# Optimization experiments

Measured on AMD Instinct MI355X. Metric: run time of the kernel, lower is better.

Reference implementation:

```python
import jax, jax.numpy as jnp
import numpy as np

B = 4096
IN_DIM = 256
OUT_DIM = 256
COND_DIM = 128
HID = 512
HYPER_OUT = IN_DIM * OUT_DIM  # 65536


def setup_inputs() -> dict:
    key = jax.random.key(0)
    ks = jax.random.split(key, 8)

    def xavier(k, shape):
        fan_in, fan_out = shape[0], shape[1]
        std = np.sqrt(2.0 / (fan_in + fan_out))
        return jax.random.normal(k, shape, dtype=jnp.float32) * std

    return {
        "input_h": jax.random.normal(ks[0], (B, IN_DIM), dtype=jnp.float32),
        "condition_z": jax.random.normal(ks[1], (B, COND_DIM), dtype=jnp.float32),
        # hypernet: Linear(COND_DIM, HID) -> ReLU -> Linear(HID, HYPER_OUT)
        "W1": xavier(ks[2], (COND_DIM, HID)),
        "b1": jnp.zeros((HID,), dtype=jnp.float32),
        "W2": xavier(ks[3], (HID, HYPER_OUT)),
        "b2": jnp.zeros((HYPER_OUT,), dtype=jnp.float32),
        # static bias (use_bias=True, generate_bias=False)
        "bias": jnp.zeros((1, OUT_DIM), dtype=jnp.float32),
    }


def reference(input_h, condition_z, W1, b1, W2, b2, bias):
    # HyperNet MLP generates per-sample weight matrix
    hyp = jax.nn.relu(condition_z @ W1 + b1)          # [B, HID]
    weight_S = hyp @ W2 + b2                          # [B, IN*OUT]  (1 GB intermediate)
    weight_S = weight_S.reshape(-1, IN_DIM, OUT_DIM)  # [B, IN, OUT]
    # batched matmul: [B,1,IN] x [B,IN,OUT] -> [B,OUT]
    out = jnp.einsum("bi,bio->bo", input_h, weight_S)
    return out + bias
```

## Files before the change

### kernel.cpp

```cpp
#include <hip/hip_runtime.h>
#include <hip/hip_bf16.h>
#include <stdint.h>


typedef _Float16 f16x8 __attribute__((ext_vector_type(8)));
typedef _Float16 f16x4 __attribute__((ext_vector_type(4)));
typedef float    f32x4 __attribute__((ext_vector_type(4)));

#define KTILES     2052
#define TILE_BYTES 32768
#define HB_OFF     (9u*1024u*1024u)
#define BP_OFF     (12u*1024u*1024u)

__global__ void k_init_out(const float* __restrict__ bias, float* __restrict__ out) {
    int idx = blockIdx.x * 256 + threadIdx.x;
    out[idx] = bias[idx & 255];
}

__global__ void k_hcast(const float* __restrict__ h, _Float16* __restrict__ hb) {
    int i = (blockIdx.x * 256 + threadIdx.x) * 8;
    f32x4 a = *(const f32x4*)(h + i);
    f32x4 b = *(const f32x4*)(h + i + 4);
    f16x8 v;
    v[0] = (_Float16)a[0]; v[1] = (_Float16)a[1]; v[2] = (_Float16)a[2]; v[3] = (_Float16)a[3];
    v[4] = (_Float16)b[0]; v[5] = (_Float16)b[1]; v[6] = (_Float16)b[2]; v[7] = (_Float16)b[3];
    *(f16x8*)(hb + i) = v;
}

__global__ void k_hypT(const float* __restrict__ z, const float* __restrict__ W1,
                       const float* __restrict__ b1, float* __restrict__ hypT) {
    int blk = blockIdx.x;
    int t   = threadIdx.x;
    if (blk == 128) {
#pragma unroll
        for (int r = 0; r < 8; ++r) hypT[(size_t)512*4096 + r*512 + t] = 1.0f;
        return;
    }
    __shared__ float zs[32][128];
    int b0 = blk * 32;
#pragma unroll
    for (int u = 0; u < 8; ++u) {
        int idx = u * 512 + t;
        zs[idx >> 7][idx & 127] = z[b0 * 128 + idx];
    }
    __syncthreads();
    float acc[32];
    float bk = b1[t];
#pragma unroll
    for (int b = 0; b < 32; ++b) acc[b] = bk;
    for (int c = 0; c < 128; ++c) {
        float w = W1[c * 512 + t];
#pragma unroll
        for (int b = 0; b < 32; ++b) acc[b] = fmaf(zs[b][c], w, acc[b]);
    }
    float* dst = hypT + (size_t)t * 4096 + b0;
#pragma unroll
    for (int v = 0; v < 8; ++v) {
        f32x4 o;
#pragma unroll
        for (int q = 0; q < 4; ++q) {
            float a = acc[v * 4 + q];
            o[q] = a > 0.f ? a : 0.f;
        }
        *(f32x4*)(dst + v * 4) = o;
    }
}

__global__ void k_pack(const float* __restrict__ W2, const float* __restrict__ b2,
                       _Float16* __restrict__ Bp) {
    __shared__ char tile[TILE_BYTES];
    int t   = blockIdx.x;
    int tid = threadIdx.x;
    long row0 = (long)t * 64;
    const float* src = (t < 2048) ? (W2 + row0 * 256) : (b2 + (row0 - 131072) * 256);
#pragma unroll
    for (int u = 0; u < 16; ++u) {
        int f = (u * 256 + tid) * 4;
        f32x4 v = *(const f32x4*)(src + f);
        int kk = f >> 8;
        int o0 = f & 255;
#pragma unroll
        for (int j = 0; j < 4; ++j) {
            int o = o0 + j;
            int addr = (o * 128 + kk * 2) ^ ((o & 7) << 4);
            *(_Float16*)(tile + addr) = (_Float16)v[j];
        }
    }
    __syncthreads();
    char* dst = (char*)Bp + (size_t)t * TILE_BYTES;
#pragma unroll
    for (int v = 0; v < 8; ++v) {
        int off = (v * 256 + tid) * 16;
        *(f32x4*)(dst + off) = *(const f32x4*)(tile + off);
    }
}

__global__ __launch_bounds__(512, 1) void k_gemm(
        const _Float16* __restrict__ hb, const float* __restrict__ hypT,
        const _Float16* __restrict__ Bp, float* __restrict__ out) {
    __shared__ char smem[114688];

    const int tid  = threadIdx.x;
    const int lane = tid & 63;
    const int wid  = tid >> 6;
    const int l15  = lane & 15, lg = lane >> 4;

    const int bid = blockIdx.x;
    const int s   = bid & 7;
    const int mt  = bid >> 3;
    const int k0  = s * 64;
    const int row_base = mt * 128;
    const int NT  = (s == 7) ? 260 : 256;

    _Float16* shyp = (_Float16*)(smem + 98304);

#pragma unroll
    for (int u = 0; u < 4; ++u) {
        int f  = (u * 512 + tid) * 4;
        int kk = f >> 7;
        int r  = f & 127;
        f32x4 v = *(const f32x4*)(hypT + (size_t)(k0 + kk) * 4096 + row_base + r);
        f16x4 o;
        o[0] = (_Float16)v[0]; o[1] = (_Float16)v[1];
        o[2] = (_Float16)v[2]; o[3] = (_Float16)v[3];
        *(f16x4*)(shyp + kk * 128 + r) = o;
    }

    auto tile_of = [&](int idx) {
        return (idx < 256) ? ((k0 + (idx & 63)) * 4 + (idx >> 6)) : (2048 + idx - 256);
    };
    auto stage = [&](int slot, int t) {
        const char* gsrc = (const char*)Bp + (size_t)t * TILE_BYTES + wid * 4096 + lane * 16;
        char* ldst = smem + slot * 32768 + wid * 4096;
#pragma unroll
        for (int q = 0; q < 4; ++q)
            __builtin_amdgcn_global_load_lds(
                (const __attribute__((address_space(1))) void*)(gsrc + q * 1024),
                (__attribute__((address_space(3))) void*)(ldst + q * 1024), 16, 0, 0);
    };

    stage(0, tile_of(0));
    stage(1, tile_of(1));
    __syncthreads();

    f32x4 acc[8][2];
#pragma unroll
    for (int i = 0; i < 8; ++i)
#pragma unroll
        for (int j = 0; j < 2; ++j)
#pragma unroll
            for (int q = 0; q < 4; ++q) acc[i][j][q] = 0.0f;

    int slot = 0;

    for (int G = 0; G < 8; ++G) {
        if (G >= 4 && s != 7) break;
        const int niter = (G < 4) ? 64 : 1;

        f16x8 af[8][2];
#pragma unroll
        for (int mf = 0; mf < 8; ++mf)
#pragma unroll
            for (int ks = 0; ks < 2; ++ks)
                af[mf][ks] = *(const f16x8*)(hb + (size_t)(row_base + mf * 16 + l15) * 256
                                             + (G & 3) * 64 + ks * 32 + lg * 8);

        for (int jj = 0; jj < niter; ++jj) {
            const int idx = (G < 4) ? G * 64 + jj : 256 + (G - 4);

            if (idx + 2 < NT) {
                int st = (slot + 2 >= 3) ? slot - 1 : slot + 2;
                stage(st, tile_of(idx + 2));
            }
            if (idx + 2 < NT)      asm volatile("s_waitcnt vmcnt(8)" ::: "memory");
            else if (idx + 1 < NT) asm volatile("s_waitcnt vmcnt(4)" ::: "memory");
            else                   asm volatile("s_waitcnt vmcnt(0)" ::: "memory");

            const char* sB = smem + slot * 32768;
            f16x8 b0[2], b1[2];
#pragma unroll
            for (int nf = 0; nf < 2; ++nf) {
                int col = wid * 32 + nf * 16 + l15;
                int swz = (col & 7) << 4;
                b0[nf] = *(const f16x8*)(sB + ((col * 128 + lg * 16) ^ swz));
                b1[nf] = *(const f16x8*)(sB + ((col * 128 + 64 + lg * 16) ^ swz));
            }
            _Float16 sch[8];
            if (idx < 256) {
#pragma unroll
                for (int mf = 0; mf < 8; ++mf)
                    sch[mf] = shyp[jj * 128 + mf * 16 + l15];
            } else {
#pragma unroll
                for (int mf = 0; mf < 8; ++mf) sch[mf] = (_Float16)1.0f;
            }

            __builtin_amdgcn_s_setprio(1);
#pragma unroll
            for (int mf = 0; mf < 8; ++mf) {
                f16x8 as0 = af[mf][0] * sch[mf];
                f16x8 as1 = af[mf][1] * sch[mf];
                acc[mf][0] = __builtin_amdgcn_mfma_f32_16x16x32_f16(as0, b0[0], acc[mf][0], 0, 0, 0);
                acc[mf][1] = __builtin_amdgcn_mfma_f32_16x16x32_f16(as0, b0[1], acc[mf][1], 0, 0, 0);
                acc[mf][0] = __builtin_amdgcn_mfma_f32_16x16x32_f16(as1, b1[0], acc[mf][0], 0, 0, 0);
                acc[mf][1] = __builtin_amdgcn_mfma_f32_16x16x32_f16(as1, b1[1], acc[mf][1], 0, 0, 0);
            }
            __builtin_amdgcn_s_setprio(0);

            slot = (slot + 1 >= 3) ? 0 : slot + 1;
        }
    }

#pragma unroll
    for (int mf = 0; mf < 8; ++mf)
#pragma unroll
        for (int nf = 0; nf < 2; ++nf) {
            int col = wid * 32 + nf * 16 + l15;
#pragma unroll
            for (int q = 0; q < 4; ++q) {
                int row = row_base + mf * 16 + lg * 4 + q;
                atomicAdd(&out[row * 256 + col], acc[mf][nf][q]);
            }
        }
}

extern "C" void kernel_launch(void* const* d_in, const int* in_sizes, int n_in,
                              void* d_out, int out_size, void* d_ws, size_t ws_size,
                              hipStream_t stream) {
    const float* h    = (const float*)d_in[0];
    const float* z    = (const float*)d_in[1];
    const float* W1   = (const float*)d_in[2];
    const float* b1   = (const float*)d_in[3];
    const float* W2   = (const float*)d_in[4];
    const float* b2   = (const float*)d_in[5];
    const float* bias = (const float*)d_in[6];
    float* out = (float*)d_out;

    float*     hypT = (float*)d_ws;
    _Float16*  hb   = (_Float16*)((char*)d_ws + HB_OFF);
    _Float16*  Bp   = (_Float16*)((char*)d_ws + BP_OFF);

    k_pack    <<<KTILES, 256, 0, stream>>>(W2, b2, Bp);
    k_hypT    <<<129,    512, 0, stream>>>(z, W1, b1, hypT);
    k_hcast   <<<512,    256, 0, stream>>>(h, hb);
    k_init_out<<<4096,   256, 0, stream>>>(bias, out);
    k_gemm    <<<256,    512, 0, stream>>>(hb, hypT, Bp, out);
}
```

Baseline: 316.2 us.

## Deepen B-tile pipeline to four stages with register double-buffered fragments

The GEMM's LDS ring grows from three to four 32KB B-tile slots, so each tile is prefetched three iterations ahead. The LDS fragments and hyp scales for the next tile are loaded into a second register set during the current MFMA block, and the shyp layout is transposed so eight scales load as one f16x8 vector. The four bias tail tiles move into a separate epilogue for the s==7 blocks. The changes aim to hide global and LDS latency behind MFMA work, at the cost of more LDS and registers; with 147KB LDS the launch-bounds hint of two blocks per CU may not be reachable.

```diff
diff --git a/kernel.cpp b/kernel.cpp
--- a/kernel.cpp
+++ b/kernel.cpp
@@ -95,10 +95,10 @@
     }
 }
 
-__global__ __launch_bounds__(512, 1) void k_gemm(
+__global__ __launch_bounds__(512, 2) void k_gemm(
         const _Float16* __restrict__ hb, const float* __restrict__ hypT,
         const _Float16* __restrict__ Bp, float* __restrict__ out) {
-    __shared__ char smem[114688];
+    __shared__ char smem[147456];
 
     const int tid  = threadIdx.x;
     const int lane = tid & 63;
@@ -112,7 +112,7 @@
     const int row_base = mt * 128;
     const int NT  = (s == 7) ? 260 : 256;
 
-    _Float16* shyp = (_Float16*)(smem + 98304);
+    _Float16* shyp = (_Float16*)(smem + 131072);
 
 #pragma unroll
     for (int u = 0; u < 4; ++u) {
@@ -120,10 +120,11 @@
         int kk = f >> 7;
         int r  = f & 127;
         f32x4 v = *(const f32x4*)(hypT + (size_t)(k0 + kk) * 4096 + row_base + r);
-        f16x4 o;
-        o[0] = (_Float16)v[0]; o[1] = (_Float16)v[1];
-        o[2] = (_Float16)v[2]; o[3] = (_Float16)v[3];
-        *(f16x4*)(shyp + kk * 128 + r) = o;
+#pragma unroll
+        for (int q = 0; q < 4; ++q) {
+            int rr = r + q;
+            shyp[kk * 128 + (rr & 15) * 8 + (rr >> 4)] = (_Float16)v[q];
+        }
     }
 
     auto tile_of = [&](int idx) {
@@ -141,6 +142,7 @@
 
     stage(0, tile_of(0));
     stage(1, tile_of(1));
+    stage(2, tile_of(2));
     __syncthreads();
 
     f32x4 acc[8][2];
@@ -151,63 +153,107 @@
 #pragma unroll
             for (int q = 0; q < 4; ++q) acc[i][j][q] = 0.0f;
 
-    int slot = 0;
-
-    for (int G = 0; G < 8; ++G) {
-        if (G >= 4 && s != 7) break;
-        const int niter = (G < 4) ? 64 : 1;
-
-        f16x8 af[8][2];
+    f16x8 one8;
+#pragma unroll
+    for (int q = 0; q < 8; ++q) one8[q] = (_Float16)1.0f;
+
+    f16x8 cA0[2], cA1[2], cB0[2], cB1[2];
+    f16x8 scA, scB;
+    f16x8 af[8][2];
+
+    {
+        const char* sB = smem;
+#pragma unroll
+        for (int nf = 0; nf < 2; ++nf) {
+            int col = wid * 32 + nf * 16 + l15;
+            int swz = (col & 7) << 4;
+            cA0[nf] = *(const f16x8*)(sB + ((col * 128 + lg * 16) ^ swz));
+            cA1[nf] = *(const f16x8*)(sB + ((col * 128 + 64 + lg * 16) ^ swz));
+        }
+        scA = *(const f16x8*)(shyp + l15 * 8);
+    }
+
+#define PIPE(C0, C1, SC, N0, N1, SN, IDX)                                                     \
+  {                                                                                           \
+    const int _i = (IDX);                                                                     \
+    if (_i + 3 < NT) stage((_i + 3) & 3, tile_of(_i + 3));                                    \
+    if (_i + 1 < NT) {                                                                        \
+      int _stg  = (_i + 3 < NT) ? _i + 3 : NT - 1;                                            \
+      int _pend = _stg - (_i + 1);                                                            \
+      if (_pend >= 2)      asm volatile("s_waitcnt vmcnt(8)" ::: "memory");                   \
+      else if (_pend == 1) asm volatile("s_waitcnt vmcnt(4)" ::: "memory");                   \
+      else                 asm volatile("s_waitcnt vmcnt(0)" ::: "memory");                   \
+      const char* _sB = smem + ((_i + 1) & 3) * 32768;                                        \
+      _Pragma("unroll")                                                                       \
+      for (int nf = 0; nf < 2; ++nf) {                                                        \
+        int col = wid * 32 + nf * 16 + l15;                                                   \
+        int swz = (col & 7) << 4;                                                             \
+        N0[nf] = *(const f16x8*)(_sB + ((col * 128 + lg * 16) ^ swz));                        \
+        N1[nf] = *(const f16x8*)(_sB + ((col * 128 + 64 + lg * 16) ^ swz));                   \
+      }                                                                                       \
+      if (_i + 1 < 256) SN = *(const f16x8*)(shyp + ((_i + 1) & 63) * 128 + l15 * 8);         \
+      else              SN = one8;                                                           \
+    }                                                                                         \
+    __builtin_amdgcn_s_setprio(1);                                                            \
+    _Pragma("unroll")                                                                         \
+    for (int mf = 0; mf < 8; ++mf) {                                                          \
+      f16x8 _a0 = C0##f(mf);                                                                  \
+      f16x8 _a1 = C1##f(mf);                                                                  \
+      acc[mf][0] = __builtin_amdgcn_mfma_f32_16x16x32_f16(_a0, C0[0], acc[mf][0], 0, 0, 0);   \
+      acc[mf][1] = __builtin_amdgcn_mfma_f32_16x16x32_f16(_a0, C0[1], acc[mf][1], 0, 0, 0);   \
+      acc[mf][0] = __builtin_amdgcn_mfma_f32_16x16x32_f16(_a1, C1[0], acc[mf][0], 0, 0, 0);   \
+      acc[mf][1] = __builtin_amdgcn_mfma_f32_16x16x32_f16(_a1, C1[1], acc[mf][1], 0, 0, 0);   \
+    }                                                                                         \
+    __builtin_amdgcn_s_setprio(0);                                                            \
+  }
+#define cA0f(mf) (af[mf][0] * scA[mf])
+#define cA1f(mf) (af[mf][1] * scA[mf])
+#define cB0f(mf) (af[mf][0] * scB[mf])
+#define cB1f(mf) (af[mf][1] * scB[mf])
+
+    for (int G = 0; G < 4; ++G) {
 #pragma unroll
         for (int mf = 0; mf < 8; ++mf)
 #pragma unroll
             for (int ks = 0; ks < 2; ++ks)
                 af[mf][ks] = *(const f16x8*)(hb + (size_t)(row_base + mf * 16 + l15) * 256
-                                             + (G & 3) * 64 + ks * 32 + lg * 8);
-
-        for (int jj = 0; jj < niter; ++jj) {
-            const int idx = (G < 4) ? G * 64 + jj : 256 + (G - 4);
-
-            if (idx + 2 < NT) {
-                int st = (slot + 2 >= 3) ? slot - 1 : slot + 2;
-                stage(st, tile_of(idx + 2));
-            }
-            if (idx + 2 < NT)      asm volatile("s_waitcnt vmcnt(8)" ::: "memory");
-            else if (idx + 1 < NT) asm volatile("s_waitcnt vmcnt(4)" ::: "memory");
-            else                   asm volatile("s_waitcnt vmcnt(0)" ::: "memory");
-
-            const char* sB = smem + slot * 32768;
-            f16x8 b0[2], b1[2];
+                                             + G * 64 + ks * 32 + lg * 8);
+
+        for (int jj = 0; jj < 64; jj += 2) {
+            const int idx = G * 64 + jj;
+            PIPE(cA0, cA1, scA, cB0, cB1, scB, idx);
+            PIPE(cB0, cB1, scB, cA0, cA1, scA, idx + 1);
+        }
+    }
+
+    if (s == 7) {
+        for (int g = 0; g < 4; ++g) {
+            int idx = 256 + g;
+            if (idx + 3 < 260) stage((idx + 3) & 3, tile_of(idx + 3));
+            asm volatile("s_waitcnt vmcnt(0)" ::: "memory");
+            f16x8 tf[8][2];
+#pragma unroll
+            for (int mf = 0; mf < 8; ++mf)
+#pragma unroll
+                for (int ks = 0; ks < 2; ++ks)
+                    tf[mf][ks] = *(const f16x8*)(hb + (size_t)(row_base + mf * 16 + l15) * 256
+                                                 + g * 64 + ks * 32 + lg * 8);
+            const char* sB = smem + (idx & 3) * 32768;
+            f16x8 t0[2], t1[2];
 #pragma unroll
             for (int nf = 0; nf < 2; ++nf) {
                 int col = wid * 32 + nf * 16 + l15;
                 int swz = (col & 7) << 4;
-                b0[nf] = *(const f16x8*)(sB + ((col * 128 + lg * 16) ^ swz));
-                b1[nf] = *(const f16x8*)(sB + ((col * 128 + 64 + lg * 16) ^ swz));
+                t0[nf] = *(const f16x8*)(sB + ((col * 128 + lg * 16) ^ swz));
+                t1[nf] = *(const f16x8*)(sB + ((col * 128 + 64 + lg * 16) ^ swz));
             }
-            _Float16 sch[8];
-            if (idx < 256) {
-#pragma unroll
-                for (int mf = 0; mf < 8; ++mf)
-                    sch[mf] = shyp[jj * 128 + mf * 16 + l15];
-            } else {
-#pragma unroll
-                for (int mf = 0; mf < 8; ++mf) sch[mf] = (_Float16)1.0f;
+#pragma unroll
+            for (int mf = 0; mf < 8; ++mf) {
+                acc[mf][0] = __builtin_amdgcn_mfma_f32_16x16x32_f16(tf[mf][0], t0[0], acc[mf][0], 0, 0, 0);
+                acc[mf][1] = __builtin_amdgcn_mfma_f32_16x16x32_f16(tf[mf][0], t0[1], acc[mf][1], 0, 0, 0);
+                acc[mf][0] = __builtin_amdgcn_mfma_f32_16x16x32_f16(tf[mf][1], t1[0], acc[mf][0], 0, 0, 0);
+                acc[mf][1] = __builtin_amdgcn_mfma_f32_16x16x32_f16(tf[mf][1], t1[1], acc[mf][1], 0, 0, 0);
             }
-
-            __builtin_amdgcn_s_setprio(1);
-#pragma unroll
-            for (int mf = 0; mf < 8; ++mf) {
-                f16x8 as0 = af[mf][0] * sch[mf];
-                f16x8 as1 = af[mf][1] * sch[mf];
-                acc[mf][0] = __builtin_amdgcn_mfma_f32_16x16x32_f16(as0, b0[0], acc[mf][0], 0, 0, 0);
-                acc[mf][1] = __builtin_amdgcn_mfma_f32_16x16x32_f16(as0, b0[1], acc[mf][1], 0, 0, 0);
-                acc[mf][0] = __builtin_amdgcn_mfma_f32_16x16x32_f16(as1, b1[0], acc[mf][0], 0, 0, 0);
-                acc[mf][1] = __builtin_amdgcn_mfma_f32_16x16x32_f16(as1, b1[1], acc[mf][1], 0, 0, 0);
-            }
-            __builtin_amdgcn_s_setprio(0);
-
-            slot = (slot + 1 >= 3) ? 0 : slot + 1;
         }
     }
 
```

After: 306.6 us. 3.0% less time.

## Switch GEMM to 32x32x16 MFMA with 4-slot pipeline and packed scaling

Applied to the files above, without the earlier changes.

Rewrites the main GEMM loop to use 32x32x16 f16 MFMA tiles instead of 16x16x32. The LDS staging buffer grows from 3 to 4 slots, and B fragments plus hyp scales are prefetched one iteration ahead via a double-buffered macro. The hyp scale is stored in LDS as duplicated packed-half pairs so A scaling runs as packed f16x2 multiplies. The bias-row tail is handled separately without scaling, which drops the ones-row from k_hypT. LDS use rises to 160KB, so the occupancy hint of 2 blocks per CU cannot actually be met, and register pressure grows.

```diff
diff --git a/kernel.cpp b/kernel.cpp
--- a/kernel.cpp
+++ b/kernel.cpp
@@ -5,7 +5,10 @@
 
 typedef _Float16 f16x8 __attribute__((ext_vector_type(8)));
 typedef _Float16 f16x4 __attribute__((ext_vector_type(4)));
+typedef _Float16 f16x2 __attribute__((ext_vector_type(2)));
 typedef float    f32x4 __attribute__((ext_vector_type(4)));
+typedef float    f32x16 __attribute__((ext_vector_type(16)));
+typedef uint32_t u32x4 __attribute__((ext_vector_type(4)));
 
 #define KTILES     2052
 #define TILE_BYTES 32768
@@ -31,11 +34,6 @@
                        const float* __restrict__ b1, float* __restrict__ hypT) {
     int blk = blockIdx.x;
     int t   = threadIdx.x;
-    if (blk == 128) {
-#pragma unroll
-        for (int r = 0; r < 8; ++r) hypT[(size_t)512*4096 + r*512 + t] = 1.0f;
-        return;
-    }
     __shared__ float zs[32][128];
     int b0 = blk * 32;
 #pragma unroll
@@ -95,15 +93,30 @@
     }
 }
 
-__global__ __launch_bounds__(512, 1) void k_gemm(
+static __device__ __forceinline__ f16x8 scale8(f16x8 a, uint32_t s) {
+    u32x4 ua = __builtin_bit_cast(u32x4, a);
+    f16x2 sv = __builtin_bit_cast(f16x2, s);
+    u32x4 r;
+#pragma unroll
+    for (int q = 0; q < 4; ++q) {
+        f16x2 aq = __builtin_bit_cast(f16x2, (uint32_t)ua[q]);
+        f16x2 rq = aq * sv;
+        r[q] = __builtin_bit_cast(uint32_t, rq);
+    }
+    return __builtin_bit_cast(f16x8, r);
+}
+
+__global__ __launch_bounds__(512, 2) void k_gemm(
         const _Float16* __restrict__ hb, const float* __restrict__ hypT,
         const _Float16* __restrict__ Bp, float* __restrict__ out) {
-    __shared__ char smem[114688];
+    __shared__ char smem[163840];
 
     const int tid  = threadIdx.x;
     const int lane = tid & 63;
     const int wid  = tid >> 6;
-    const int l15  = lane & 15, lg = lane >> 4;
+    const int l31  = lane & 31;
+    const int hsel = lane >> 5;
+    const int colb = wid * 32 + l31;
 
     const int bid = blockIdx.x;
     const int s   = bid & 7;
@@ -112,7 +125,7 @@
     const int row_base = mt * 128;
     const int NT  = (s == 7) ? 260 : 256;
 
-    _Float16* shyp = (_Float16*)(smem + 98304);
+    uint32_t* shyp32 = (uint32_t*)(smem + 131072);
 
 #pragma unroll
     for (int u = 0; u < 4; ++u) {
@@ -120,10 +133,13 @@
         int kk = f >> 7;
         int r  = f & 127;
         f32x4 v = *(const f32x4*)(hypT + (size_t)(k0 + kk) * 4096 + row_base + r);
-        f16x4 o;
-        o[0] = (_Float16)v[0]; o[1] = (_Float16)v[1];
-        o[2] = (_Float16)v[2]; o[3] = (_Float16)v[3];
-        *(f16x4*)(shyp + kk * 128 + r) = o;
+#pragma unroll
+        for (int q = 0; q < 4; ++q) {
+            int rr = r + q;
+            _Float16 hf = (_Float16)v[q];
+            uint32_t d  = (uint32_t)__builtin_bit_cast(uint16_t, hf) * 0x10001u;
+            shyp32[kk * 128 + (rr & 31) * 4 + (rr >> 5)] = d;
+        }
     }
 
     auto tile_of = [&](int idx) {
@@ -141,86 +157,106 @@
 
     stage(0, tile_of(0));
     stage(1, tile_of(1));
+    stage(2, tile_of(2));
     __syncthreads();
 
-    f32x4 acc[8][2];
-#pragma unroll
-    for (int i = 0; i < 8; ++i)
-#pragma unroll
-        for (int j = 0; j < 2; ++j)
-#pragma unroll
-            for (int q = 0; q < 4; ++q) acc[i][j][q] = 0.0f;
-
-    int slot = 0;
-
-    for (int G = 0; G < 8; ++G) {
-        if (G >= 4 && s != 7) break;
-        const int niter = (G < 4) ? 64 : 1;
-
-        f16x8 af[8][2];
-#pragma unroll
-        for (int mf = 0; mf < 8; ++mf)
-#pragma unroll
-            for (int ks = 0; ks < 2; ++ks)
-                af[mf][ks] = *(const f16x8*)(hb + (size_t)(row_base + mf * 16 + l15) * 256
-                                             + (G & 3) * 64 + ks * 32 + lg * 8);
-
-        for (int jj = 0; jj < niter; ++jj) {
-            const int idx = (G < 4) ? G * 64 + jj : 256 + (G - 4);
-
-            if (idx + 2 < NT) {
-                int st = (slot + 2 >= 3) ? slot - 1 : slot + 2;
-                stage(st, tile_of(idx + 2));
-            }
-            if (idx + 2 < NT)      asm volatile("s_waitcnt vmcnt(8)" ::: "memory");
-            else if (idx + 1 < NT) asm volatile("s_waitcnt vmcnt(4)" ::: "memory");
-            else                   asm volatile("s_waitcnt vmcnt(0)" ::: "memory");
-
-            const char* sB = smem + slot * 32768;
-            f16x8 b0[2], b1[2];
-#pragma unroll
-            for (int nf = 0; nf < 2; ++nf) {
-                int col = wid * 32 + nf * 16 + l15;
-                int swz = (col & 7) << 4;
-                b0[nf] = *(const f16x8*)(sB + ((col * 128 + lg * 16) ^ swz));
-                b1[nf] = *(const f16x8*)(sB + ((col * 128 + 64 + lg * 16) ^ swz));
-            }
-            _Float16 sch[8];
-            if (idx < 256) {
-#pragma unroll
-                for (int mf = 0; mf < 8; ++mf)
-                    sch[mf] = shyp[jj * 128 + mf * 16 + l15];
-            } else {
-#pragma unroll
-                for (int mf = 0; mf < 8; ++mf) sch[mf] = (_Float16)1.0f;
-            }
-
-            __builtin_amdgcn_s_setprio(1);
-#pragma unroll
-            for (int mf = 0; mf < 8; ++mf) {
-                f16x8 as0 = af[mf][0] * sch[mf];
-                f16x8 as1 = af[mf][1] * sch[mf];
-                acc[mf][0] = __builtin_amdgcn_mfma_f32_16x16x32_f16(as0, b0[0], acc[mf][0], 0, 0, 0);
-                acc[mf][1] = __builtin_amdgcn_mfma_f32_16x16x32_f16(as0, b0[1], acc[mf][1], 0, 0, 0);
-                acc[mf][0] = __builtin_amdgcn_mfma_f32_16x16x32_f16(as1, b1[0], acc[mf][0], 0, 0, 0);
-                acc[mf][1] = __builtin_amdgcn_mfma_f32_16x16x32_f16(as1, b1[1], acc[mf][1], 0, 0, 0);
-            }
-            __builtin_amdgcn_s_setprio(0);
-
-            slot = (slot + 1 >= 3) ? 0 : slot + 1;
-        }
-    }
-
-#pragma unroll
-    for (int mf = 0; mf < 8; ++mf)
-#pragma unroll
-        for (int nf = 0; nf < 2; ++nf) {
-            int col = wid * 32 + nf * 16 + l15;
-#pragma unroll
-            for (int q = 0; q < 4; ++q) {
-                int row = row_base + mf * 16 + lg * 4 + q;
-                atomicAdd(&out[row * 256 + col], acc[mf][nf][q]);
-            }
+    int boffs[4];
+#pragma unroll
+    for (int ks = 0; ks < 4; ++ks)
+        boffs[ks] = (colb * 128 + ks * 32 + hsel * 16) ^ ((colb & 7) << 4);
+    const int soff = l31 * 4;
+
+    f32x16 acc[4];
+#pragma unroll
+    for (int i = 0; i < 4; ++i)
+#pragma unroll
+        for (int q = 0; q < 16; ++q) acc[i][q] = 0.0f;
+
+    const u32x4 oneD = {0x3C003C00u, 0x3C003C00u, 0x3C003C00u, 0x3C003C00u};
+
+    f16x8 bC[4], bN[4];
+    u32x4 sdC, sdN;
+    f16x8 af[4][4];
+
+    {
+        const char* sB = smem;
+#pragma unroll
+        for (int ks = 0; ks < 4; ++ks) bC[ks] = *(const f16x8*)(sB + boffs[ks]);
+        sdC = *(const u32x4*)(shyp32 + soff);
+    }
+
+#define PIPE(BC, SDC_, BN, SDN_, IDX)                                                        \
+  {                                                                                          \
+    const int _i = (IDX);                                                                    \
+    if (_i + 3 < NT) stage((_i + 3) & 3, tile_of(_i + 3));                                   \
+    if (_i + 1 < NT) {                                                                       \
+      int _stg  = (_i + 3 < NT) ? _i + 3 : NT - 1;                                           \
+      int _pend = _stg - (_i + 1);                                                           \
+      if (_pend >= 2)      asm volatile("s_waitcnt vmcnt(8)" ::: "memory");                  \
+      else if (_pend == 1) asm volatile("s_waitcnt vmcnt(4)" ::: "memory");                  \
+      else                 asm volatile("s_waitcnt vmcnt(0)" ::: "memory");                  \
+      const char* _sB = smem + ((_i + 1) & 3) * 32768;                                       \
+      _Pragma("unroll")                                                                      \
+      for (int ks = 0; ks < 4; ++ks) BN[ks] = *(const f16x8*)(_sB + boffs[ks]);              \
+      SDN_ = (_i + 1 < 256) ? *(const u32x4*)(shyp32 + ((_i + 1) & 63) * 128 + soff) : oneD; \
+    }                                                                                        \
+    __builtin_amdgcn_s_setprio(1);                                                           \
+    _Pragma("unroll")                                                                        \
+    for (int m = 0; m < 4; ++m) {                                                            \
+      uint32_t _sd = SDC_[m];                                                                \
+      _Pragma("unroll")                                                                      \
+      for (int ks = 0; ks < 4; ++ks)                                                         \
+        acc[m] = __builtin_amdgcn_mfma_f32_32x32x16_f16(scale8(af[m][ks], _sd), BC[ks],      \
+                                                        acc[m], 0, 0, 0);                    \
+    }                                                                                        \
+    __builtin_amdgcn_s_setprio(0);                                                           \
+  }
+
+    for (int G = 0; G < 4; ++G) {
+#pragma unroll
+        for (int m = 0; m < 4; ++m)
+#pragma unroll
+            for (int ks = 0; ks < 4; ++ks)
+                af[m][ks] = *(const f16x8*)(hb + (size_t)(row_base + m * 32 + l31) * 256
+                                            + G * 64 + ks * 16 + hsel * 8);
+
+        for (int jj = 0; jj < 64; jj += 2) {
+            const int idx = G * 64 + jj;
+            PIPE(bC, sdC, bN, sdN, idx);
+            PIPE(bN, sdN, bC, sdC, idx + 1);
+        }
+    }
+
+    if (s == 7) {
+        for (int g = 0; g < 4; ++g) {
+            int idx = 256 + g;
+            if (idx + 3 < 260) stage((idx + 3) & 3, tile_of(idx + 3));
+#pragma unroll
+            for (int m = 0; m < 4; ++m)
+#pragma unroll
+                for (int ks = 0; ks < 4; ++ks)
+                    af[m][ks] = *(const f16x8*)(hb + (size_t)(row_base + m * 32 + l31) * 256
+                                                + g * 64 + ks * 16 + hsel * 8);
+            asm volatile("s_waitcnt vmcnt(0)" ::: "memory");
+            const char* sB = smem + (idx & 3) * 32768;
+            f16x8 tB[4];
+#pragma unroll
+            for (int ks = 0; ks < 4; ++ks) tB[ks] = *(const f16x8*)(sB + boffs[ks]);
+#pragma unroll
+            for (int m = 0; m < 4; ++m)
+#pragma unroll
+                for (int ks = 0; ks < 4; ++ks)
+                    acc[m] = __builtin_amdgcn_mfma_f32_32x32x16_f16(af[m][ks], tB[ks],
+                                                                    acc[m], 0, 0, 0);
+        }
+    }
+
+#pragma unroll
+    for (int m = 0; m < 4; ++m)
+#pragma unroll
+        for (int reg = 0; reg < 16; ++reg) {
+            int row = row_base + m * 32 + hsel * 4 + (reg & 3) + 8 * (reg >> 2);
+            atomicAdd(&out[row * 256 + colb], acc[m][reg]);
         }
 }
 
@@ -241,7 +277,7 @@
     _Float16*  Bp   = (_Float16*)((char*)d_ws + BP_OFF);
 
     k_pack    <<<KTILES, 256, 0, stream>>>(W2, b2, Bp);
-    k_hypT    <<<129,    512, 0, stream>>>(z, W1, b1, hypT);
+    k_hypT    <<<128,    512, 0, stream>>>(z, W1, b1, hypT);
     k_hcast   <<<512,    256, 0, stream>>>(h, hb);
     k_init_out<<<4096,   256, 0, stream>>>(bias, out);
     k_gemm    <<<256,    512, 0, stream>>>(hb, hypT, Bp, out);
```

Measured after the change: 333.6 us. 5.5% more time.

## Split GEMM N across blocks and ping-pong two wave groups over tiles

Applied to the files above, without the earlier changes.

The gemm grid doubles to 512 blocks. Each block now covers half the output columns, and two blocks can share a CU under launch_bounds(512,2) with a smaller LDS footprint. Inside a block, two 4-wave groups handle alternating K tiles through a 4-slot LDS ring. The hyp scale vector is stored transposed so it loads as one f16x8, and the ones-row in hypT is dropped in favour of an unscaled bias pass. Each block still loads the full A fragments, so A traffic doubles. The more complex cross-group staging also risks synchronisation hazards, since it relies on waitcnt with no barrier between the two groups.

```diff
diff --git a/kernel.cpp b/kernel.cpp
--- a/kernel.cpp
+++ b/kernel.cpp
@@ -4,7 +4,6 @@
 
 
 typedef _Float16 f16x8 __attribute__((ext_vector_type(8)));
-typedef _Float16 f16x4 __attribute__((ext_vector_type(4)));
 typedef float    f32x4 __attribute__((ext_vector_type(4)));
 
 #define KTILES     2052
@@ -31,11 +30,6 @@
                        const float* __restrict__ b1, float* __restrict__ hypT) {
     int blk = blockIdx.x;
     int t   = threadIdx.x;
-    if (blk == 128) {
-#pragma unroll
-        for (int r = 0; r < 8; ++r) hypT[(size_t)512*4096 + r*512 + t] = 1.0f;
-        return;
-    }
     __shared__ float zs[32][128];
     int b0 = blk * 32;
 #pragma unroll
@@ -95,24 +89,28 @@
     }
 }
 
-__global__ __launch_bounds__(512, 1) void k_gemm(
+__global__ __launch_bounds__(512, 2) void k_gemm(
         const _Float16* __restrict__ hb, const float* __restrict__ hypT,
         const _Float16* __restrict__ Bp, float* __restrict__ out) {
-    __shared__ char smem[114688];
+    __shared__ char smem[81920];
 
     const int tid  = threadIdx.x;
     const int lane = tid & 63;
     const int wid  = tid >> 6;
     const int l15  = lane & 15, lg = lane >> 4;
-
-    const int bid = blockIdx.x;
-    const int s   = bid & 7;
-    const int mt  = bid >> 3;
-    const int k0  = s * 64;
+    const int p    = wid >> 2;
+    const int wn   = wid & 3;
+
+    const int bid  = blockIdx.x;
+    const int s    = bid & 7;
+    const int rest = bid >> 3;
+    const int nt   = rest & 1;
+    const int mt   = rest >> 1;
+    const int k0   = s * 64;
     const int row_base = mt * 128;
-    const int NT  = (s == 7) ? 260 : 256;
-
-    _Float16* shyp = (_Float16*)(smem + 98304);
+    const int NT   = (s == 7) ? 260 : 256;
+
+    _Float16* shyp = (_Float16*)(smem + 65536);
 
 #pragma unroll
     for (int u = 0; u < 4; ++u) {
@@ -120,18 +118,21 @@
         int kk = f >> 7;
         int r  = f & 127;
         f32x4 v = *(const f32x4*)(hypT + (size_t)(k0 + kk) * 4096 + row_base + r);
-        f16x4 o;
-        o[0] = (_Float16)v[0]; o[1] = (_Float16)v[1];
-        o[2] = (_Float16)v[2]; o[3] = (_Float16)v[3];
-        *(f16x4*)(shyp + kk * 128 + r) = o;
+#pragma unroll
+        for (int q = 0; q < 4; ++q) {
+            int rr = r + q;
+            shyp[kk * 128 + (rr & 15) * 8 + (rr >> 4)] = (_Float16)v[q];
+        }
     }
 
     auto tile_of = [&](int idx) {
         return (idx < 256) ? ((k0 + (idx & 63)) * 4 + (idx >> 6)) : (2048 + idx - 256);
     };
-    auto stage = [&](int slot, int t) {
-        const char* gsrc = (const char*)Bp + (size_t)t * TILE_BYTES + wid * 4096 + lane * 16;
-        char* ldst = smem + slot * 32768 + wid * 4096;
+    auto stage = [&](int idx) {
+        int t = tile_of(idx);
+        const char* gsrc = (const char*)Bp + (size_t)t * TILE_BYTES + (nt << 14)
+                         + wn * 4096 + lane * 16;
+        char* ldst = smem + (idx & 3) * 16384 + wn * 4096;
 #pragma unroll
         for (int q = 0; q < 4; ++q)
             __builtin_amdgcn_global_load_lds(
@@ -139,8 +140,7 @@
                 (__attribute__((address_space(3))) void*)(ldst + q * 1024), 16, 0, 0);
     };
 
-    stage(0, tile_of(0));
-    stage(1, tile_of(1));
+    stage(p);
     __syncthreads();
 
     f32x4 acc[8][2];
@@ -151,63 +151,111 @@
 #pragma unroll
             for (int q = 0; q < 4; ++q) acc[i][j][q] = 0.0f;
 
-    int slot = 0;
-
-    for (int G = 0; G < 8; ++G) {
-        if (G >= 4 && s != 7) break;
-        const int niter = (G < 4) ? 64 : 1;
-
-        f16x8 af[8][2];
-#pragma unroll
-        for (int mf = 0; mf < 8; ++mf)
-#pragma unroll
-            for (int ks = 0; ks < 2; ++ks)
-                af[mf][ks] = *(const f16x8*)(hb + (size_t)(row_base + mf * 16 + l15) * 256
-                                             + (G & 3) * 64 + ks * 32 + lg * 8);
-
-        for (int jj = 0; jj < niter; ++jj) {
-            const int idx = (G < 4) ? G * 64 + jj : 256 + (G - 4);
-
-            if (idx + 2 < NT) {
-                int st = (slot + 2 >= 3) ? slot - 1 : slot + 2;
-                stage(st, tile_of(idx + 2));
-            }
-            if (idx + 2 < NT)      asm volatile("s_waitcnt vmcnt(8)" ::: "memory");
-            else if (idx + 1 < NT) asm volatile("s_waitcnt vmcnt(4)" ::: "memory");
-            else                   asm volatile("s_waitcnt vmcnt(0)" ::: "memory");
-
-            const char* sB = smem + slot * 32768;
-            f16x8 b0[2], b1[2];
-#pragma unroll
-            for (int nf = 0; nf < 2; ++nf) {
-                int col = wid * 32 + nf * 16 + l15;
-                int swz = (col & 7) << 4;
-                b0[nf] = *(const f16x8*)(sB + ((col * 128 + lg * 16) ^ swz));
-                b1[nf] = *(const f16x8*)(sB + ((col * 128 + 64 + lg * 16) ^ swz));
-            }
-            _Float16 sch[8];
-            if (idx < 256) {
-#pragma unroll
-                for (int mf = 0; mf < 8; ++mf)
-                    sch[mf] = shyp[jj * 128 + mf * 16 + l15];
-            } else {
-#pragma unroll
-                for (int mf = 0; mf < 8; ++mf) sch[mf] = (_Float16)1.0f;
-            }
-
-            __builtin_amdgcn_s_setprio(1);
+    int boff0[2];
+#pragma unroll
+    for (int nf = 0; nf < 2; ++nf) {
+        int col = wn * 32 + nf * 16 + l15;
+        boff0[nf] = (col * 128 + lg * 16) ^ ((col & 7) << 4);
+    }
+
+    f16x8 af[8][2];
+#pragma unroll
+    for (int mf = 0; mf < 8; ++mf)
+#pragma unroll
+        for (int ks = 0; ks < 2; ++ks)
+            af[mf][ks] = *(const f16x8*)(hb + (size_t)(row_base + mf * 16 + l15) * 256
+                                         + ks * 32 + lg * 8);
+
+#define READF(B00, B01, B10, B11, SC, IDX)                                                    \
+    {                                                                                         \
+      const char* _sB = smem + ((IDX) & 3) * 16384;                                           \
+      B00 = *(const f16x8*)(_sB + boff0[0]);                                                  \
+      B01 = *(const f16x8*)(_sB + boff0[1]);                                                  \
+      B10 = *(const f16x8*)(_sB + (boff0[0] ^ 64));                                           \
+      B11 = *(const f16x8*)(_sB + (boff0[1] ^ 64));                                           \
+      SC  = *(const f16x8*)(shyp + ((IDX) & 63) * 128 + l15 * 8);                             \
+    }
+
+#define MF4(MF0, SC, B00, B01, B10, B11)                                                      \
+    __builtin_amdgcn_s_setprio(1);                                                            \
+    _Pragma("unroll")                                                                         \
+    for (int mf = MF0; mf < MF0 + 4; ++mf) {                                                  \
+      f16x8 _a0 = af[mf][0] * SC[mf];                                                         \
+      f16x8 _a1 = af[mf][1] * SC[mf];                                                         \
+      acc[mf][0] = __builtin_amdgcn_mfma_f32_16x16x32_f16(_a0, B00, acc[mf][0], 0, 0, 0);     \
+      acc[mf][1] = __builtin_amdgcn_mfma_f32_16x16x32_f16(_a0, B01, acc[mf][1], 0, 0, 0);     \
+      acc[mf][0] = __builtin_amdgcn_mfma_f32_16x16x32_f16(_a1, B10, acc[mf][0], 0, 0, 0);     \
+      acc[mf][1] = __builtin_amdgcn_mfma_f32_16x16x32_f16(_a1, B11, acc[mf][1], 0, 0, 0);     \
+    }                                                                                         \
+    __builtin_amdgcn_s_setprio(0);
+
+#define STAGE_WAIT(IDX)                                                                       \
+    {                                                                                         \
+      asm volatile("s_waitcnt lgkmcnt(0)" ::: "memory");      \
+      if ((IDX) + 2 < NT) {                                                                   \
+        stage((IDX) + 2);                                                                     \
+        asm volatile("s_waitcnt vmcnt(4)" ::: "memory");                                      \
+      } else {                                                                                \
+        asm volatile("s_waitcnt vmcnt(0)" ::: "memory");                                      \
+      }                                                                                       \
+    }
+
+    for (int G = 0; G < 4; ++G) {
+        if (G > 0) {
+#pragma unroll
+            for (int mf = 0; mf < 8; ++mf)
+#pragma unroll
+                for (int ks = 0; ks < 2; ++ks)
+                    af[mf][ks] = *(const f16x8*)(hb + (size_t)(row_base + mf * 16 + l15) * 256
+                                                 + G * 64 + ks * 32 + lg * 8);
+        }
+        if (p == 0) {
+            for (int jj = 0; jj < 64; jj += 2) {
+                const int idx = G * 64 + jj;
+                STAGE_WAIT(idx);
+                f16x8 b00, b01, b10, b11, sc;
+                READF(b00, b01, b10, b11, sc, idx);
+                MF4(0, sc, b00, b01, b10, b11);
+                MF4(4, sc, b00, b01, b10, b11);
+            }
+        } else {
+            for (int jj = 1; jj < 64; jj += 2) {
+                const int idx = G * 64 + jj;
+                f16x8 b00, b01, b10, b11, sc;
+                READF(b00, b01, b10, b11, sc, idx);
+                MF4(0, sc, b00, b01, b10, b11);
+                __builtin_amdgcn_sched_barrier(0);
+                asm volatile("s_waitcnt lgkmcnt(0)" ::: "memory");
+                if (idx + 2 < NT) stage(idx + 2);
+                __builtin_amdgcn_sched_barrier(0);
+                MF4(4, sc, b00, b01, b10, b11);
+                asm volatile("s_waitcnt vmcnt(0)" ::: "memory");
+            }
+        }
+    }
+
+    if (s == 7) {
+        for (int m = p; m < 4; m += 2) {
+            const int idx = 256 + m;
+#pragma unroll
+            for (int mf = 0; mf < 8; ++mf)
+#pragma unroll
+                for (int ks = 0; ks < 2; ++ks)
+                    af[mf][ks] = *(const f16x8*)(hb + (size_t)(row_base + mf * 16 + l15) * 256
+                                                 + m * 64 + ks * 32 + lg * 8);
+            STAGE_WAIT(idx);
+            const char* sB = smem + (idx & 3) * 16384;
+            f16x8 b00 = *(const f16x8*)(sB + boff0[0]);
+            f16x8 b01 = *(const f16x8*)(sB + boff0[1]);
+            f16x8 b10 = *(const f16x8*)(sB + (boff0[0] ^ 64));
+            f16x8 b11 = *(const f16x8*)(sB + (boff0[1] ^ 64));
 #pragma unroll
             for (int mf = 0; mf < 8; ++mf) {
-                f16x8 as0 = af[mf][0] * sch[mf];
-                f16x8 as1 = af[mf][1] * sch[mf];
-                acc[mf][0] = __builtin_amdgcn_mfma_f32_16x16x32_f16(as0, b0[0], acc[mf][0], 0, 0, 0);
-                acc[mf][1] = __builtin_amdgcn_mfma_f32_16x16x32_f16(as0, b0[1], acc[mf][1], 0, 0, 0);
-                acc[mf][0] = __builtin_amdgcn_mfma_f32_16x16x32_f16(as1, b1[0], acc[mf][0], 0, 0, 0);
-                acc[mf][1] = __builtin_amdgcn_mfma_f32_16x16x32_f16(as1, b1[1], acc[mf][1], 0, 0, 0);
-            }
-            __builtin_amdgcn_s_setprio(0);
-
-            slot = (slot + 1 >= 3) ? 0 : slot + 1;
+                acc[mf][0] = __builtin_amdgcn_mfma_f32_16x16x32_f16(af[mf][0], b00, acc[mf][0], 0, 0, 0);
+                acc[mf][1] = __builtin_amdgcn_mfma_f32_16x16x32_f16(af[mf][0], b01, acc[mf][1], 0, 0, 0);
+                acc[mf][0] = __builtin_amdgcn_mfma_f32_16x16x32_f16(af[mf][1], b10, acc[mf][0], 0, 0, 0);
+                acc[mf][1] = __builtin_amdgcn_mfma_f32_16x16x32_f16(af[mf][1], b11, acc[mf][1], 0, 0, 0);
+            }
         }
     }
 
@@ -215,7 +263,7 @@
     for (int mf = 0; mf < 8; ++mf)
 #pragma unroll
         for (int nf = 0; nf < 2; ++nf) {
-            int col = wid * 32 + nf * 16 + l15;
+            int col = nt * 128 + wn * 32 + nf * 16 + l15;
 #pragma unroll
             for (int q = 0; q < 4; ++q) {
                 int row = row_base + mf * 16 + lg * 4 + q;
@@ -241,8 +289,8 @@
     _Float16*  Bp   = (_Float16*)((char*)d_ws + BP_OFF);
 
     k_pack    <<<KTILES, 256, 0, stream>>>(W2, b2, Bp);
-    k_hypT    <<<129,    512, 0, stream>>>(z, W1, b1, hypT);
+    k_hypT    <<<128,    512, 0, stream>>>(z, W1, b1, hypT);
     k_hcast   <<<512,    256, 0, stream>>>(h, hb);
     k_init_out<<<4096,   256, 0, stream>>>(bias, out);
-    k_gemm    <<<256,    512, 0, stream>>>(hb, hypT, Bp, out);
-}
+    k_gemm    <<<512,    512, 0, stream>>>(hb, hypT, Bp, out);
+}
```

After: 330.9 us. +4.6%, slower.
